# Performance work log

Measured on AMD Instinct MI355X. Metric: run time of the kernel, lower is better.

Reference implementation:

```python
import jax, jax.numpy as jnp
import numpy as np

SHIFT = 1  # fixed shift_direction (module draws +/-1 at random; we pin +1)

def setup_inputs() -> dict:
    key = jax.random.key(0)
    kx, kw = jax.random.split(key)
    x = jax.random.normal(kx, (1024, 256, 7, 7), dtype=jnp.float32)
    W = jax.random.normal(kw, (128, 3, 3, 512), dtype=jnp.float32)
    return {"x": x, "W": W}

def _fwd(x, W):
    B = x.shape[0]
    t = x.reshape(B, 256, 7, 7)
    # unfold((3,1), padding=(1,0)) along H: t[b,c,k,h,w] = x_pad[b,c,h+k-1,w]
    xp = jnp.pad(t, ((0, 0), (0, 0), (1, 1), (0, 0)))
    t = jnp.stack([xp[:, :, k:k + 7, :] for k in range(3)], axis=2)  # (B,256,3,7,7)
    t = t.reshape(B, 2, 128, 3, 7, 7).transpose(0, 2, 3, 4, 1, 5)   # (B,128,3,7,2,7)
    t = t.reshape(B, 128, 3, 14, 7)
    t = jnp.roll(t, SHIFT, axis=3)
    t = t.reshape(B, 128, 3, 7, 2, 7).sum(axis=4)                   # (B,128,3,7,7)
    t = t.transpose(0, 1, 3, 2, 4)                                  # (B,128,7,3,7)
    t = jnp.roll(t, SHIFT, axis=4)
    # second unfold((3,1), padding=(1,0)) along W dim: gather 3 shifted slices
    tp = jnp.pad(t, ((0, 0), (0, 0), (0, 0), (0, 0), (1, 1)))
    t3 = jnp.stack([tp[..., k2:k2 + 7] for k2 in range(3)], axis=-1)  # (B,128,7,3,7,3) = (m,l,n,j,o,k)
    out = jnp.einsum('mlnjok,ljki->mnoi', t3, W)                     # (B,7,7,512)
    return out.transpose(0, 3, 1, 2)                                 # (B,512,7,7)

def reference(x, W):
    return _fwd(x, W)
```

## Files before the change

### kernel.cpp

```cpp
#include <hip/hip_runtime.h>

typedef __attribute__((ext_vector_type(8)))  __bf16 bvec8;
typedef __attribute__((ext_vector_type(4)))  __bf16 bvec4;
typedef __attribute__((ext_vector_type(16))) float  fvec16;
typedef __attribute__((ext_vector_type(8)))  short  svec8;

__global__ __launch_bounds__(256) void pack_w(const float* __restrict__ W,
                                              __bf16* __restrict__ Wp) {
    int u = blockIdx.x * 256 + threadIdx.x;
    if (u >= 73728) return;
    int lane = u & 63;
    int f    = (u >> 6) & 7;
    int wi   = (u >> 9) & 3;
    int t    = u >> 11;
    int am = f & 3, h = f >> 2;
    int i  = ((wi * 4 + am) << 5) + (lane & 31);
    int K0 = ((2 * t + h) << 4) + ((lane >> 5) << 3);
    bvec8 o;
#pragma unroll
    for (int e = 0; e < 8; ++e) {
        int K  = K0 + e;
        int jk = K >> 7;
        int l  = K & 127;
        int j  = (jk * 11) >> 5;
        int k  = jk - 3 * j;
        o[e] = (__bf16)W[((l * 9 + j * 3 + k) << 9) + i];
    }
    *(bvec8*)&Wp[(size_t)u * 8] = o;
}

__global__ __launch_bounds__(512, 2) void conv_mfma(
    const float* __restrict__ x, const __bf16* __restrict__ Wp,
    float* __restrict__ out)
{
    __shared__ __align__(16) char smem[65024];
    __bf16* xs = (__bf16*)smem;
    __bf16* ys = (__bf16*)(smem + 25088);
    float*  T  = (float*)smem;

    const int tid  = threadIdx.x;
    const int lane = tid & 63;
    const int l31  = lane & 31;
    const int ls5  = lane >> 5;
    const int wid  = tid >> 6;
    const int wi   = wid & 3;
    const int ws   = wid >> 2;
    const int b0   = blockIdx.x * 2;

    const float* xb  = x + (size_t)b0 * 12544;
    const char*  WpB = (const char*)Wp;

    bvec8 aE[4][2], aO[4][2];
    {
        const char* g0 = WpB + (size_t)wi * 8192 + ((size_t)lane << 4);
#pragma unroll
        for (int am = 0; am < 4; ++am)
#pragma unroll
            for (int h = 0; h < 2; ++h) {
                aE[am][h] = *(const bvec8*)(g0 + ((h * 4 + am) << 10));
                aO[am][h] = *(const bvec8*)(g0 + 32768 + ((h * 4 + am) << 10));
            }
    }

#pragma unroll
    for (int bb = 0; bb < 2; ++bb) {
        for (int it = 0; it < 7; ++it) {
            int e4 = it * 512 + tid;
            if (e4 < 3136) {
                const float4 v = ((const float4*)(xb + bb * 12544))[e4];
                bvec4 pk = { (__bf16)v.x, (__bf16)v.y, (__bf16)v.z, (__bf16)v.w };
                *(bvec4*)&xs[e4 * 4] = pk;
            }
        }
        __syncthreads();
        for (int it = 0; it < 3; ++it) {
            int up = it * 512 + tid;
            if (up < 1248) {
                int row  = up >> 4;
                int useg = up & 15;
                int l0   = useg * 8;
                bvec8 ov;
                if (row == 77) {
                    ov = __builtin_bit_cast(bvec8, (svec8)0);
                } else if (row < 63) {
                    int t = row / 7, w = row - t * 7;
                    int tb = t + 5; if (tb >= 7) tb -= 7;
                    int cB = tb * 7 + w;
                    bool mA = (t >= 1) && (t <= 7);
                    int cA = mA ? (t - 1) * 7 + w : 0;
#pragma unroll
                    for (int d = 0; d < 8; ++d) {
                        float fa = mA ? (float)xs[(l0 + d) * 49 + cA] : 0.f;
                        float fb = (float)xs[(128 + l0 + d) * 49 + cB];
                        ov[d] = (__bf16)(fa + fb);
                    }
                } else if (row < 70) {
                    int w = row - 63;
#pragma unroll
                    for (int d = 0; d < 8; ++d) ov[d] = xs[(l0 + d) * 49 + w];
                } else {
                    int w = row - 70;
#pragma unroll
                    for (int d = 0; d < 8; ++d) ov[d] = xs[(l0 + d) * 49 + 7 + w];
                }
                *(bvec8*)&ys[((bb * 78 + row) << 7) + ((useg ^ (row & 15)) << 3)] = ov;
            }
        }
        __syncthreads();
    }

    const int s_ = ws * 32 + l31;
    const int sc = (s_ < 49) ? s_ : 48;
    const int nq = sc / 7;
    const int oo = sc - nq * 7;

    fvec16 acc[4][2];
#pragma unroll
    for (int am = 0; am < 4; ++am)
#pragma unroll
        for (int bb = 0; bb < 2; ++bb)
#pragma unroll
            for (int r = 0; r < 16; ++r) acc[am][bb][r] = 0.f;

#define GEO(JK, ROWE, RX) {                                                   \
        int j_ = ((JK) * 11) >> 5; int k_ = (JK) - 3 * j_;                    \
        int tw_ = oo + k_ + 5; int w_ = tw_ >= 7 ? tw_ - 7 : tw_;             \
        int row_ = (nq + j_) * 7 + w_;                                        \
        if (nq == 1 && j_ == 0) row_ = 63 + w_;                               \
        if (nq == 0 && j_ == 2) row_ = 70 + w_;                               \
        if ((k_ == 0 && oo == 0) || (k_ == 2 && oo == 6)) row_ = 77;          \
        ROWE = row_ << 7; RX = row_ & 15; }

#define READF(DST, P, ROWE, RX) {                                             \
        _Pragma("unroll")                                                     \
        for (int h_ = 0; h_ < 2; ++h_) {                                      \
            int u_ = ((P) * 4 + h_ * 2 + ls5) ^ (RX);                         \
            DST[0][h_] = *(const bvec8*)&ys[(ROWE) + (u_ << 3)];              \
            DST[1][h_] = *(const bvec8*)&ys[9984 + (ROWE) + (u_ << 3)]; } }

#define MFMA16(AW, BF) {                                                      \
        __builtin_amdgcn_s_setprio(1);                                        \
        _Pragma("unroll")                                                     \
        for (int h_ = 0; h_ < 2; ++h_)                                        \
        _Pragma("unroll")                                                     \
        for (int am_ = 0; am_ < 4; ++am_)                                     \
        _Pragma("unroll")                                                     \
        for (int bb_ = 0; bb_ < 2; ++bb_)                                     \
            acc[am_][bb_] = __builtin_amdgcn_mfma_f32_32x32x16_bf16(          \
                AW[am_][h_], BF[bb_][h_], acc[am_][bb_], 0, 0, 0);            \
        __builtin_amdgcn_s_setprio(0); }

#define PREFW(AW, TT) {                                                       \
        const char* gp_ = WpB + (size_t)((TT) * 4 + wi) * 8192                \
                          + ((size_t)lane << 4);                              \
        _Pragma("unroll")                                                     \
        for (int am_ = 0; am_ < 4; ++am_)                                     \
        _Pragma("unroll")                                                     \
        for (int h_ = 0; h_ < 2; ++h_)                                        \
            AW[am_][h_] = *(const bvec8*)(gp_ + ((h_ * 4 + am_) << 10)); }

    int rowE, rx, rowEn, rxn;
    GEO(0, rowE, rx);
    bvec8 bfA[2][2], bfB[2][2];
    READF(bfA, 0, rowE, rx);

    for (int jk = 0; jk < 9; ++jk) {
        READF(bfB, 1, rowE, rx);
        MFMA16(aE, bfA);
        PREFW(aE, 4 * jk + 2);
        READF(bfA, 2, rowE, rx);
        MFMA16(aO, bfB);
        PREFW(aO, 4 * jk + 3);
        { int jn = jk < 8 ? jk + 1 : 8; GEO(jn, rowEn, rxn); }
        READF(bfB, 3, rowE, rx);
        MFMA16(aE, bfA);
        if (jk < 8) PREFW(aE, 4 * jk + 4);
        READF(bfA, 0, rowEn, rxn);
        MFMA16(aO, bfB);
        if (jk < 8) PREFW(aO, 4 * jk + 5);
        rowE = rowEn; rx = rxn;
    }

#undef GEO
#undef READF
#undef MFMA16
#undef PREFW

#pragma unroll
    for (int pass = 0; pass < 4; ++pass) {
        const int bb = pass >> 1, ih = pass & 1;
        __syncthreads();
        if ((wi >> 1) == ih && s_ < 49) {
            const int irb = (wi & 1) * 128 + 4 * ls5;
#pragma unroll
            for (int am = 0; am < 4; ++am)
#pragma unroll
                for (int r = 0; r < 16; ++r) {
                    int ir = irb + am * 32 + (r & 3) + 8 * (r >> 2);
                    T[ir * 52 + s_] = acc[am][bb][r];
                }
        }
        __syncthreads();
        const size_t ob = (size_t)(b0 + bb) * 25088 + (size_t)ih * 12544;
        for (int it = 0; it < 25; ++it) {
            int idx = it * 512 + tid;
            if (idx < 12544) {
                int ir = idx / 49;
                int s  = idx - ir * 49;
                out[ob + idx] = T[ir * 52 + s];
            }
        }
    }
}

extern "C" void kernel_launch(void* const* d_in, const int* in_sizes, int n_in,
                              void* d_out, int out_size, void* d_ws, size_t ws_size,
                              hipStream_t stream) {
    const float* x = (const float*)d_in[0];
    const float* W = (const float*)d_in[1];
    float* out = (float*)d_out;
    __bf16* Wp = (__bf16*)d_ws;
    (void)in_sizes; (void)n_in; (void)out_size; (void)ws_size;

    hipLaunchKernelGGL(pack_w, dim3(288), dim3(256), 0, stream, W, Wp);
    hipLaunchKernelGGL(conv_mfma, dim3(512), dim3(512), 0, stream, x, Wp, out);
}
```

Baseline: 102.2 us.

## Re-tile warps over output channels, stage both batches at once, store directly

```diff
diff --git a/kernel.cpp b/kernel.cpp
--- a/kernel.cpp
+++ b/kernel.cpp
@@ -10,11 +10,11 @@
     int u = blockIdx.x * 256 + threadIdx.x;
     if (u >= 73728) return;
     int lane = u & 63;
-    int f    = (u >> 6) & 7;
-    int wi   = (u >> 9) & 3;
+    int f    = (u >> 6) & 3;
+    int wd   = (u >> 8) & 7;
     int t    = u >> 11;
-    int am = f & 3, h = f >> 2;
-    int i  = ((wi * 4 + am) << 5) + (lane & 31);
+    int am = f & 1, h = f >> 1;
+    int i  = (wd << 6) + (am << 5) + (lane & 31);
     int K0 = ((2 * t + h) << 4) + ((lane >> 5) << 3);
     bvec8 o;
 #pragma unroll
@@ -33,152 +33,163 @@
     const float* __restrict__ x, const __bf16* __restrict__ Wp,
     float* __restrict__ out)
 {
-    __shared__ __align__(16) char smem[65024];
+    extern __shared__ __align__(16) char smem[];
     __bf16* xs = (__bf16*)smem;
-    __bf16* ys = (__bf16*)(smem + 25088);
-    float*  T  = (float*)smem;
+    __bf16* ys = (__bf16*)(smem + 50176);
 
     const int tid  = threadIdx.x;
     const int lane = tid & 63;
     const int l31  = lane & 31;
     const int ls5  = lane >> 5;
-    const int wid  = tid >> 6;
-    const int wi   = wid & 3;
-    const int ws   = wid >> 2;
+    const int wd   = tid >> 6;
     const int b0   = blockIdx.x * 2;
 
     const float* xb  = x + (size_t)b0 * 12544;
     const char*  WpB = (const char*)Wp;
-
-    bvec8 aE[4][2], aO[4][2];
-    {
-        const char* g0 = WpB + (size_t)wi * 8192 + ((size_t)lane << 4);
-#pragma unroll
-        for (int am = 0; am < 4; ++am)
-#pragma unroll
-            for (int h = 0; h < 2; ++h) {
-                aE[am][h] = *(const bvec8*)(g0 + ((h * 4 + am) << 10));
-                aO[am][h] = *(const bvec8*)(g0 + 32768 + ((h * 4 + am) << 10));
+    const int wbase  = wd * 4096 + lane * 16;
+
+    bvec8 aE[2][2], aO[2][2];
+#pragma unroll
+    for (int am = 0; am < 2; ++am)
+#pragma unroll
+        for (int h = 0; h < 2; ++h) {
+            aE[am][h] = *(const bvec8*)(WpB + wbase + ((h * 2 + am) << 10));
+            aO[am][h] = *(const bvec8*)(WpB + 32768 + wbase + ((h * 2 + am) << 10));
+        }
+
+    for (int it = 0; it < 13; ++it) {
+        int e4 = it * 512 + tid;
+        if (e4 < 6272) {
+            const float4 v = ((const float4*)xb)[e4];
+            bvec4 pk = { (__bf16)v.x, (__bf16)v.y, (__bf16)v.z, (__bf16)v.w };
+            *(bvec4*)&xs[e4 * 4] = pk;
+        }
+    }
+    __syncthreads();
+
+    for (int it = 0; it < 5; ++it) {
+        int up = it * 512 + tid;
+        if (up < 2496) {
+            int bb   = up >= 1248;
+            int rem  = up - bb * 1248;
+            int row  = rem >> 4;
+            int useg = rem & 15;
+            int l0   = useg * 8;
+            const __bf16* xsb = xs + bb * 12544;
+            bvec8 ov;
+            if (row == 77) {
+                ov = __builtin_bit_cast(bvec8, (svec8)0);
+            } else if (row < 63) {
+                int t = row / 7, w = row - t * 7;
+                int tb = t + 5; if (tb >= 7) tb -= 7;
+                int cB = tb * 7 + w;
+                bool mA = (t >= 1) && (t <= 7);
+                int cA = mA ? (t - 1) * 7 + w : 0;
+#pragma unroll
+                for (int d = 0; d < 8; ++d) {
+                    float fa = mA ? (float)xsb[(l0 + d) * 49 + cA] : 0.f;
+                    float fb = (float)xsb[(128 + l0 + d) * 49 + cB];
+                    ov[d] = (__bf16)(fa + fb);
+                }
+            } else if (row < 70) {
+                int w = row - 63;
+#pragma unroll
+                for (int d = 0; d < 8; ++d) ov[d] = xsb[(l0 + d) * 49 + w];
+            } else {
+                int w = row - 70;
+#pragma unroll
+                for (int d = 0; d < 8; ++d) ov[d] = xsb[(l0 + d) * 49 + 7 + w];
             }
-    }
-
-#pragma unroll
-    for (int bb = 0; bb < 2; ++bb) {
-        for (int it = 0; it < 7; ++it) {
-            int e4 = it * 512 + tid;
-            if (e4 < 3136) {
-                const float4 v = ((const float4*)(xb + bb * 12544))[e4];
-                bvec4 pk = { (__bf16)v.x, (__bf16)v.y, (__bf16)v.z, (__bf16)v.w };
-                *(bvec4*)&xs[e4 * 4] = pk;
-            }
-        }
-        __syncthreads();
-        for (int it = 0; it < 3; ++it) {
-            int up = it * 512 + tid;
-            if (up < 1248) {
-                int row  = up >> 4;
-                int useg = up & 15;
-                int l0   = useg * 8;
-                bvec8 ov;
-                if (row == 77) {
-                    ov = __builtin_bit_cast(bvec8, (svec8)0);
-                } else if (row < 63) {
-                    int t = row / 7, w = row - t * 7;
-                    int tb = t + 5; if (tb >= 7) tb -= 7;
-                    int cB = tb * 7 + w;
-                    bool mA = (t >= 1) && (t <= 7);
-                    int cA = mA ? (t - 1) * 7 + w : 0;
-#pragma unroll
-                    for (int d = 0; d < 8; ++d) {
-                        float fa = mA ? (float)xs[(l0 + d) * 49 + cA] : 0.f;
-                        float fb = (float)xs[(128 + l0 + d) * 49 + cB];
-                        ov[d] = (__bf16)(fa + fb);
-                    }
-                } else if (row < 70) {
-                    int w = row - 63;
-#pragma unroll
-                    for (int d = 0; d < 8; ++d) ov[d] = xs[(l0 + d) * 49 + w];
-                } else {
-                    int w = row - 70;
-#pragma unroll
-                    for (int d = 0; d < 8; ++d) ov[d] = xs[(l0 + d) * 49 + 7 + w];
-                }
-                *(bvec8*)&ys[((bb * 78 + row) << 7) + ((useg ^ (row & 15)) << 3)] = ov;
-            }
-        }
-        __syncthreads();
-    }
-
-    const int s_ = ws * 32 + l31;
-    const int sc = (s_ < 49) ? s_ : 48;
-    const int nq = sc / 7;
-    const int oo = sc - nq * 7;
-
-    fvec16 acc[4][2];
-#pragma unroll
-    for (int am = 0; am < 4; ++am)
-#pragma unroll
-        for (int bb = 0; bb < 2; ++bb)
-#pragma unroll
-            for (int r = 0; r < 16; ++r) acc[am][bb][r] = 0.f;
+            *(bvec8*)&ys[((bb * 78 + row) << 7) + ((useg ^ (row & 15)) << 3)] = ov;
+        }
+    }
+
+    int nq[2], oo[2];
+#pragma unroll
+    for (int sn = 0; sn < 2; ++sn) {
+        int s = sn * 32 + l31;
+        int sc = (s < 49) ? s : 48;
+        nq[sn] = sc / 7;
+        oo[sn] = sc - nq[sn] * 7;
+    }
+
+    fvec16 acc[2][2][2];
+#pragma unroll
+    for (int am = 0; am < 2; ++am)
+#pragma unroll
+        for (int sn = 0; sn < 2; ++sn)
+#pragma unroll
+            for (int bb = 0; bb < 2; ++bb)
+#pragma unroll
+                for (int r = 0; r < 16; ++r) acc[am][sn][bb][r] = 0.f;
+
+    __syncthreads();
 
 #define GEO(JK, ROWE, RX) {                                                   \
         int j_ = ((JK) * 11) >> 5; int k_ = (JK) - 3 * j_;                    \
-        int tw_ = oo + k_ + 5; int w_ = tw_ >= 7 ? tw_ - 7 : tw_;             \
-        int row_ = (nq + j_) * 7 + w_;                                        \
-        if (nq == 1 && j_ == 0) row_ = 63 + w_;                               \
-        if (nq == 0 && j_ == 2) row_ = 70 + w_;                               \
-        if ((k_ == 0 && oo == 0) || (k_ == 2 && oo == 6)) row_ = 77;          \
-        ROWE = row_ << 7; RX = row_ & 15; }
+        _Pragma("unroll")                                                     \
+        for (int sn_ = 0; sn_ < 2; ++sn_) {                                   \
+            int tw_ = oo[sn_] + k_ + 5; int w_ = tw_ >= 7 ? tw_ - 7 : tw_;    \
+            int row_ = (nq[sn_] + j_) * 7 + w_;                               \
+            if (nq[sn_] == 1 && j_ == 0) row_ = 63 + w_;                      \
+            if (nq[sn_] == 0 && j_ == 2) row_ = 70 + w_;                      \
+            if ((k_ == 0 && oo[sn_] == 0) || (k_ == 2 && oo[sn_] == 6))       \
+                row_ = 77;                                                    \
+            ROWE[sn_] = row_ << 7; RX[sn_] = row_ & 15; } }
 
 #define READF(DST, P, ROWE, RX) {                                             \
         _Pragma("unroll")                                                     \
+        for (int sn_ = 0; sn_ < 2; ++sn_)                                     \
+        _Pragma("unroll")                                                     \
         for (int h_ = 0; h_ < 2; ++h_) {                                      \
-            int u_ = ((P) * 4 + h_ * 2 + ls5) ^ (RX);                         \
-            DST[0][h_] = *(const bvec8*)&ys[(ROWE) + (u_ << 3)];              \
-            DST[1][h_] = *(const bvec8*)&ys[9984 + (ROWE) + (u_ << 3)]; } }
+            int u_ = ((P) * 4 + h_ * 2 + ls5) ^ RX[sn_];                      \
+            DST[sn_][0][h_] = *(const bvec8*)&ys[ROWE[sn_] + (u_ << 3)];      \
+            DST[sn_][1][h_] = *(const bvec8*)&ys[9984 + ROWE[sn_] + (u_ << 3)]; } }
 
 #define MFMA16(AW, BF) {                                                      \
         __builtin_amdgcn_s_setprio(1);                                        \
         _Pragma("unroll")                                                     \
         for (int h_ = 0; h_ < 2; ++h_)                                        \
         _Pragma("unroll")                                                     \
-        for (int am_ = 0; am_ < 4; ++am_)                                     \
+        for (int am_ = 0; am_ < 2; ++am_)                                     \
+        _Pragma("unroll")                                                     \
+        for (int sn_ = 0; sn_ < 2; ++sn_)                                     \
         _Pragma("unroll")                                                     \
         for (int bb_ = 0; bb_ < 2; ++bb_)                                     \
-            acc[am_][bb_] = __builtin_amdgcn_mfma_f32_32x32x16_bf16(          \
-                AW[am_][h_], BF[bb_][h_], acc[am_][bb_], 0, 0, 0);            \
+            acc[am_][sn_][bb_] = __builtin_amdgcn_mfma_f32_32x32x16_bf16(     \
+                AW[am_][h_], BF[sn_][bb_][h_], acc[am_][sn_][bb_], 0, 0, 0);  \
         __builtin_amdgcn_s_setprio(0); }
 
 #define PREFW(AW, TT) {                                                       \
-        const char* gp_ = WpB + (size_t)((TT) * 4 + wi) * 8192                \
-                          + ((size_t)lane << 4);                              \
-        _Pragma("unroll")                                                     \
-        for (int am_ = 0; am_ < 4; ++am_)                                     \
+        const char* gp_ = WpB + ((size_t)(TT) << 15) + wbase;                 \
+        _Pragma("unroll")                                                     \
+        for (int am_ = 0; am_ < 2; ++am_)                                     \
         _Pragma("unroll")                                                     \
         for (int h_ = 0; h_ < 2; ++h_)                                        \
-            AW[am_][h_] = *(const bvec8*)(gp_ + ((h_ * 4 + am_) << 10)); }
-
-    int rowE, rx, rowEn, rxn;
+            AW[am_][h_] = *(const bvec8*)(gp_ + ((h_ * 2 + am_) << 10)); }
+
+    int rowE[2], rx[2], rowEn[2], rxn[2];
     GEO(0, rowE, rx);
-    bvec8 bfA[2][2], bfB[2][2];
+    bvec8 bfA[2][2][2], bfB[2][2][2];
     READF(bfA, 0, rowE, rx);
 
     for (int jk = 0; jk < 9; ++jk) {
+        const int t0 = jk * 4;
         READF(bfB, 1, rowE, rx);
         MFMA16(aE, bfA);
-        PREFW(aE, 4 * jk + 2);
+        PREFW(aE, t0 + 2);
         READF(bfA, 2, rowE, rx);
         MFMA16(aO, bfB);
-        PREFW(aO, 4 * jk + 3);
+        PREFW(aO, t0 + 3);
         { int jn = jk < 8 ? jk + 1 : 8; GEO(jn, rowEn, rxn); }
         READF(bfB, 3, rowE, rx);
         MFMA16(aE, bfA);
-        if (jk < 8) PREFW(aE, 4 * jk + 4);
+        if (jk < 8) PREFW(aE, t0 + 4);
         READF(bfA, 0, rowEn, rxn);
         MFMA16(aO, bfB);
-        if (jk < 8) PREFW(aO, 4 * jk + 5);
-        rowE = rowEn; rx = rxn;
+        if (jk < 8) PREFW(aO, t0 + 5);
+#pragma unroll
+        for (int sn = 0; sn < 2; ++sn) { rowE[sn] = rowEn[sn]; rx[sn] = rxn[sn]; }
     }
 
 #undef GEO
@@ -187,27 +198,20 @@
 #undef PREFW
 
 #pragma unroll
-    for (int pass = 0; pass < 4; ++pass) {
-        const int bb = pass >> 1, ih = pass & 1;
-        __syncthreads();
-        if ((wi >> 1) == ih && s_ < 49) {
-            const int irb = (wi & 1) * 128 + 4 * ls5;
-#pragma unroll
-            for (int am = 0; am < 4; ++am)
+    for (int am = 0; am < 2; ++am) {
+        const int i0 = wd * 64 + am * 32 + 4 * ls5;
+#pragma unroll
+        for (int sn = 0; sn < 2; ++sn) {
+            if (sn == 1 && l31 >= 17) continue;
+            const int s = sn * 32 + l31;
+#pragma unroll
+            for (int bb = 0; bb < 2; ++bb) {
+                const size_t ob = (size_t)(b0 + bb) * 25088;
 #pragma unroll
                 for (int r = 0; r < 16; ++r) {
-                    int ir = irb + am * 32 + (r & 3) + 8 * (r >> 2);
-                    T[ir * 52 + s_] = acc[am][bb][r];
+                    int i = i0 + (r & 3) + 8 * (r >> 2);
+                    out[ob + (size_t)i * 49 + s] = acc[am][sn][bb][r];
                 }
-        }
-        __syncthreads();
-        const size_t ob = (size_t)(b0 + bb) * 25088 + (size_t)ih * 12544;
-        for (int it = 0; it < 25; ++it) {
-            int idx = it * 512 + tid;
-            if (idx < 12544) {
-                int ir = idx / 49;
-                int s  = idx - ir * 49;
-                out[ob + idx] = T[ir * 52 + s];
             }
         }
     }
@@ -222,6 +226,9 @@
     __bf16* Wp = (__bf16*)d_ws;
     (void)in_sizes; (void)n_in; (void)out_size; (void)ws_size;
 
+    hipFuncSetAttribute(reinterpret_cast<const void*>(conv_mfma),
+                        hipFuncAttributeMaxDynamicSharedMemorySize, 90112);
+
     hipLaunchKernelGGL(pack_w, dim3(288), dim3(256), 0, stream, W, Wp);
-    hipLaunchKernelGGL(conv_mfma, dim3(512), dim3(512), 0, stream, x, Wp, out);
+    hipLaunchKernelGGL(conv_mfma, dim3(512), dim3(512), 90112, stream, x, Wp, out);
 }
```

Result: faster. 94.55 us (-7.5%).
